# Performance work log

Measured on AMD Instinct MI355X. Metric: run time of the kernel, lower is better.

The kernel has to match this reference:

```python
import jax, jax.numpy as jnp
import numpy as np

B, T, I, H, O = 32, 2048, 12, 512, 3
L = 3  # GRU layers


def _gru_layer(x_seq, h0, w_ih, w_hh, b_ih, b_hh):
    # x_seq: [B,T,D], h0: [B,H]; PyTorch gate order: r, z, n
    xW = jnp.einsum('btd,gd->btg', x_seq, w_ih) + b_ih  # [B,T,3H]

    def step(h, xw_t):
        hw = h @ w_hh.T + b_hh                  # [B,3H]
        xr, xz, xn = jnp.split(xw_t, 3, axis=-1)
        hr, hz, hn = jnp.split(hw, 3, axis=-1)
        r = jax.nn.sigmoid(xr + hr)
        z = jax.nn.sigmoid(xz + hz)
        n = jnp.tanh(xn + r * hn)
        h_new = (1.0 - z) * n + z * h
        return h_new, h_new

    h_last, ys = jax.lax.scan(step, h0, jnp.swapaxes(xW, 0, 1))  # ys: [T,B,H]
    return jnp.swapaxes(ys, 0, 1), h_last


def _prelu(x, a):
    return jnp.where(x >= 0, x, a * x)


def setup_inputs() -> dict:
    key = jax.random.key(0)
    ks = jax.random.split(key, 40)
    s = 1.0 / np.sqrt(H)

    def u(k, shape):
        return jax.random.uniform(k, shape, jnp.float32, -s, s)

    inp = {
        'x': jax.random.normal(ks[0], (B, T, I), jnp.float32),
        'vel_init': jax.random.normal(ks[1], (B, 1, 3), jnp.float32),
    }
    in_dims = [I, H, H]
    for l in range(L):
        inp[f'w_ih_{l}'] = u(ks[2 + 4 * l], (3 * H, in_dims[l]))
        inp[f'w_hh_{l}'] = u(ks[3 + 4 * l], (3 * H, H))
        inp[f'b_ih_{l}'] = u(ks[4 + 4 * l], (3 * H,))
        inp[f'b_hh_{l}'] = u(ks[5 + 4 * l], (3 * H,))
    inp['a1'] = jnp.array([0.25], jnp.float32)  # PReLU (single shared param)
    inp['dec_in_w'] = u(ks[14], (H, I)); inp['dec_in_b'] = u(ks[15], (H,))
    inp['vd0_w'] = u(ks[16], (H, 3)); inp['vd0_b'] = u(ks[17], (H,))
    inp['vd1_w'] = u(ks[18], (H, 3)); inp['vd1_b'] = u(ks[19], (H,))
    inp['vd2_w'] = u(ks[20], (H, 3)); inp['vd2_b'] = u(ks[21], (H,))
    inp['vel_w'] = u(ks[22], (O, H)); inp['vel_b'] = u(ks[23], (O,))
    inp['std_w'] = u(ks[24], (O, H)); inp['std_b'] = u(ks[25], (O,))
    inp['attn_w'] = u(ks[26], (1, H)); inp['attn_b'] = u(ks[27], (1,))
    return inp


def reference(x, vel_init, w_ih_0, w_hh_0, b_ih_0, b_hh_0,
              w_ih_1, w_hh_1, b_ih_1, b_hh_1,
              w_ih_2, w_hh_2, b_ih_2, b_hh_2,
              a1, dec_in_w, dec_in_b,
              vd0_w, vd0_b, vd1_w, vd1_b, vd2_w, vd2_b,
              vel_w, vel_b, std_w, std_b, attn_w, attn_b):
    v0 = vel_init[:, 0, :]  # [B,3]
    # h0 per layer from velocity decoders (permute(1,0,2)+cat -> layer axis)
    h0s = [v0 @ vd0_w.T + vd0_b, v0 @ vd1_w.T + vd1_b, v0 @ vd2_w.T + vd2_b]
    w_ih = [w_ih_0, w_ih_1, w_ih_2]
    w_hh = [w_hh_0, w_hh_1, w_hh_2]
    b_ih = [b_ih_0, b_ih_1, b_ih_2]
    b_hh = [b_hh_0, b_hh_1, b_hh_2]

    out = x
    for l in range(L):
        out, _ = _gru_layer(out, h0s[l], w_ih[l], w_hh[l], b_ih[l], b_hh[l])

    out = _prelu(out, a1)
    # softmax skip-attention over time dim
    scores = jnp.einsum('bth,oh->bto', out, attn_w) + attn_b      # [B,T,1]
    attn = jax.nn.softmax(scores, axis=1)
    out = out + attn * (jnp.einsum('bti,hi->bth', x, dec_in_w) + dec_in_b)

    vel = jnp.einsum('bth,oh->bto', out, vel_w) + vel_b
    std = jnp.einsum('bth,oh->bto', out, std_w) + std_b
    return vel, std
```

## Files before the change

### kernel.cpp

```cpp
#include <hip/hip_runtime.h>
#include <stdint.h>


#define B_ 32
#define T_ 2048
#define H_ 512
#define R_ 128

typedef __attribute__((ext_vector_type(8))) short s8v;
typedef __attribute__((ext_vector_type(4))) float f4v;
typedef __attribute__((ext_vector_type(4))) uint32_t u32x4;
typedef __attribute__((ext_vector_type(2))) unsigned short u16x2;

__device__ __forceinline__ uint16_t f2bf(float f){ return __builtin_bit_cast(uint16_t, (__bf16)f); }
__device__ __forceinline__ float bf2f(uint16_t b){ return __builtin_bit_cast(float, ((uint32_t)b)<<16); }

__device__ __forceinline__ s8v pack8(const float* f){
  s8v r;
  #pragma unroll
  for (int i=0;i<8;++i) r[i] = (short)f2bf(f[i]);
  return r;
}
__device__ __forceinline__ f4v mfma16(s8v a, s8v b, f4v c){
  return __builtin_amdgcn_mfma_f32_16x16x32_bf16(a,b,c,0,0,0);
}
#if __has_builtin(__builtin_amdgcn_rcpf)
__device__ __forceinline__ float rcp_(float x){ return __builtin_amdgcn_rcpf(x); }
#else
__device__ __forceinline__ float rcp_(float x){ return 1.0f/x; }
#endif
__device__ __forceinline__ float sigm(float s){ return rcp_(1.f + __expf(-s)); }
__device__ __forceinline__ float tanh2(float v){ return 1.f - 2.f*rcp_(1.f + __expf(2.f*v)); }

__device__ __forceinline__ u32x4 load_x4_sc(const void* p){
  u32x4 r;
  asm volatile("global_load_dwordx4 %0, %1, off sc0 sc1" : "=v"(r) : "v"(p) : "memory");
  return r;
}
__device__ __forceinline__ uint32_t load_u32_sc_wait(const void* p){
  uint32_t r;
  asm volatile("global_load_dword %0, %1, off sc0 sc1\n\ts_waitcnt vmcnt(0)"
               : "=v"(r) : "v"(p) : "memory");
  return r;
}
__device__ __forceinline__ void store_s16_sc(void* p, uint32_t v){
  asm volatile("global_store_short %0, %1, off sc0 sc1" :: "v"(p), "v"(v) : "memory");
}
__device__ __forceinline__ void store_u32_sc(void* p, uint32_t v){
  asm volatile("global_store_dword %0, %1, off sc0 sc1" :: "v"(p), "v"(v) : "memory");
}

__device__ __forceinline__ bool valid16(const u32x4* a){
  u16x2 m = {0, 0};
  #pragma unroll
  for (int c=0;c<16;++c){
    #pragma unroll
    for (int i=0;i<4;++i)
      m = __builtin_elementwise_max(m, __builtin_bit_cast(u16x2, a[c][i]));
  }
  unsigned short mm = (m[0] > m[1]) ? m[0] : m[1];
  return mm != (unsigned short)0xFFFFu;
}

__global__ void poison_kernel(uint32_t* p, unsigned int n16)
{
  u32x4 v = {0xFFFFFFFFu, 0xFFFFFFFFu, 0xFFFFFFFFu, 0xFFFFFFFFu};
  for (unsigned int k = blockIdx.x*blockDim.x + threadIdx.x; k < n16;
       k += gridDim.x*blockDim.x)
    ((u32x4*)p)[k] = v;
}

__global__ void init_kernel(const float* __restrict__ vel_init,
    const float* __restrict__ w0, const float* __restrict__ b0,
    const float* __restrict__ w1, const float* __restrict__ b1,
    const float* __restrict__ w2, const float* __restrict__ b2,
    float* __restrict__ h0f, uint16_t* __restrict__ h0b, uint32_t* progress)
{
  const int l = blockIdx.x, tid = threadIdx.x;
  const float* w  = (l==0)?w0:((l==1)?w1:w2);
  const float* bb = (l==0)?b0:((l==1)?b1:b2);
  for (int idx = tid; idx < B_*H_; idx += 256){
    int b = idx >> 9, j = idx & 511;
    float s = bb[j] + vel_init[b*3+0]*w[j*3+0] + vel_init[b*3+1]*w[j*3+1]
                    + vel_init[b*3+2]*w[j*3+2];
    h0f[(size_t)l*(B_*H_) + idx] = s;
    h0b[(size_t)l*(B_*H_) + idx] = f2bf(s);
  }
  if (l == 0 && tid < 192) progress[tid] = 0;
}

struct ScanParams {
  const float* x;
  const float* wih[3];
  const float* whh[3];
  const float* bih[3];
  const float* bhh[3];
  const float* h0f;
  const uint16_t* h0b;
  uint16_t* ring0;
  uint16_t* ring1;
  uint16_t* out2;
  uint32_t* progress;
};

__global__ __launch_bounds__(128, 1) void fused_scan(ScanParams P)
{
  const int tid  = threadIdx.x;
  const int lane = tid & 63;
  const int mt   = tid >> 6;
  const int wgid = blockIdx.x;
  const int layer = wgid >> 5;
  const int wg   = wgid & 31;
  const int j0   = wg * 16;
  const int u    = lane & 15;
  const int lq   = lane >> 4;
  const int ko   = lq * 8;
  const int bd   = lq * 4;

  __shared__ uint16_t lds[48*512];

  const float* wih = P.wih[layer];
  const float* whh = P.whh[layer];
  const float* bih = P.bih[layer];
  const float* bhh = P.bhh[layer];

  const float bs0 = bih[0*H_ + j0 + u] + bhh[0*H_ + j0 + u];
  const float bs1 = bih[1*H_ + j0 + u] + bhh[1*H_ + j0 + u];
  const float bi2 = bih[2*H_ + j0 + u];
  const float bh2 = bhh[2*H_ + j0 + u];

  s8v whhf[3][16];
  #pragma unroll
  for (int nt=0; nt<3; ++nt){
    #pragma unroll
    for (int ks=0; ks<16; ++ks){
      const float* wp = whh + (size_t)(nt*H_ + j0 + u)*H_ + ks*32 + ko;
      float tmp[8];
      #pragma unroll
      for (int i=0;i<8;++i) tmp[i] = wp[i];
      whhf[nt][ks] = pack8(tmp);
    }
  }

  s8v w0f[3];
  if (layer == 0){
    #pragma unroll
    for (int nt=0; nt<3; ++nt){
      float tmp[8];
      #pragma unroll
      for (int i=0;i<8;++i){
        int k = ko + i;
        tmp[i] = (k < 12) ? wih[(size_t)(nt*H_ + j0 + u)*12 + k] : 0.f;
      }
      w0f[nt] = pack8(tmp);
    }
  } else {
    for (int e = tid; e < (48*512)/8; e += 128) {
      int idx = e * 8;
      int g = idx >> 9, k = idx & 511;
      const float* wp = wih + (size_t)((g>>4)*H_ + j0 + (g&15))*H_ + k;
      float tmp[8];
      #pragma unroll
      for (int i=0;i<8;++i) tmp[i] = wp[i];
      s8v v = pack8(tmp);
      uint32_t msk = (uint32_t)((((g&7) ^ (((g>>3)&1)<<1))) << 4);
      uint32_t off = (uint32_t)g*1024u + ((((uint32_t)k)*2u) ^ msk);
      *(u32x4*)((char*)lds + off) = __builtin_bit_cast(u32x4, v);
    }
  }
  __syncthreads();

  const uint16_t* inring = (layer==1) ? P.ring0 : P.ring1;
  uint16_t* outbuf = (layer==0) ? P.ring0 : ((layer==1) ? P.ring1 : P.out2);
  const bool outlin = (layer == 2);
  uint32_t* myprog = P.progress + layer*64 + wg*2 + mt;
  const uint32_t* nextprog = (layer<2) ? (P.progress + (layer+1)*64) : nullptr;

  float hold[4];
  #pragma unroll
  for (int r=0;r<4;++r)
    hold[r] = P.h0f[(size_t)layer*(B_*H_) + (size_t)(mt*16 + bd + r)*H_ + j0 + u];

  const uint32_t sw  = (uint32_t)((((u&7) ^ (((u>>3)&1)<<1))) << 4);
  const uint32_t gb0 = (uint32_t)((0*16 + u) * 1024);
  const uint32_t gb1 = (uint32_t)((1*16 + u) * 1024);
  const uint32_t gb2 = (uint32_t)((2*16 + u) * 1024);
  const uint32_t koB = (uint32_t)(ko * 2);

  int poison_until = R_/2 + 60;

  for (int t = 0; t < T_; ++t) {
    f4v ac0 = {0,0,0,0}, ac1 = {0,0,0,0}, axn = {0,0,0,0}, ahn = {0,0,0,0};

    if (layer == 0) {
      const float* xp = P.x + ((size_t)(mt*16 + u)*T_ + (size_t)t)*12;
      float4 lo  = *(const float4*)(xp);
      float4 md  = *(const float4*)(xp + 4);
      float4 hi4 = *(const float4*)(xp + 8);
      float xv[8];
      xv[0] = (ko==0) ? lo.x : hi4.x;  xv[1] = (ko==0) ? lo.y : hi4.y;
      xv[2] = (ko==0) ? lo.z : hi4.z;  xv[3] = (ko==0) ? lo.w : hi4.w;
      xv[4] = (ko==0) ? md.x : 0.f;    xv[5] = (ko==0) ? md.y : 0.f;
      xv[6] = (ko==0) ? md.z : 0.f;    xv[7] = (ko==0) ? md.w : 0.f;
      s8v a = pack8(xv);
      ac0 = mfma16(a, w0f[0], ac0);
      ac1 = mfma16(a, w0f[1], ac1);
      axn = mfma16(a, w0f[2], axn);
    }

    if (layer < 2 && t >= R_/2) {
      if (t > poison_until) {
        while (1) {
          int c = (int)load_u32_sc_wait(nextprog + lane);
          #pragma unroll
          for (int off=32; off>0; off>>=1){
            int c2 = __shfl_xor(c, off, 64);
            c = (c2 < c) ? c2 : c;
          }
          poison_until = c + R_/2 - 4;
          if (t <= poison_until) break;
          __builtin_amdgcn_s_sleep(8);
        }
      }
      int sp = (t + R_/2) & (R_-1);
      uint16_t* prow = outbuf + (size_t)sp*(B_*H_) + (size_t)(mt*16 + bd)*H_ + j0 + u;
      #pragma unroll
      for (int r=0;r<4;++r) store_s16_sc(prow + (size_t)r*H_, 0xFFFFu);
    }

    if (layer > 0 && (t & 15) == 15 && lane == 0)
      store_u32_sc(myprog, (uint32_t)t);

    u32x4 xa[16], ha[16];
    bool xok = (layer == 0);
    bool hok = (t == 0);
    const uint16_t* hp = ((t == 0)
        ? (P.h0b + (size_t)layer*(B_*H_))
        : (outlin ? (P.out2 + (size_t)(t-1)*(B_*H_))
                  : (outbuf + (size_t)((t-1) & (R_-1))*(B_*H_))))
        + (size_t)(mt*16+u)*H_ + ko;
    const uint16_t* xin = (layer > 0)
        ? (inring + (size_t)(t & (R_-1))*(B_*H_) + (size_t)(mt*16+u)*H_ + ko)
        : nullptr;

    #pragma unroll
    for (int ks=0; ks<16; ++ks) ha[ks] = load_x4_sc(hp + ks*32);
    if (layer > 0) {
      #pragma unroll
      for (int ks=0; ks<16; ++ks) xa[ks] = load_x4_sc(xin + ks*32);
    }
    asm volatile("s_waitcnt vmcnt(0)" ::: "memory");
    __builtin_amdgcn_sched_barrier(0);
    if (!hok) hok = (__ballot(valid16(ha)) == ~0ull);
    if (!xok) xok = (__ballot(valid16(xa)) == ~0ull);

    while (!xok) {
      #pragma unroll
      for (int ks=0; ks<16; ++ks) xa[ks] = load_x4_sc(xin + ks*32);
      if (!hok) {
        #pragma unroll
        for (int ks=0; ks<16; ++ks) ha[ks] = load_x4_sc(hp + ks*32);
      }
      asm volatile("s_waitcnt vmcnt(0)" ::: "memory");
      __builtin_amdgcn_sched_barrier(0);
      xok = (__ballot(valid16(xa)) == ~0ull);
      if (!hok) hok = (__ballot(valid16(ha)) == ~0ull);
    }

    if (layer > 0) {
      #pragma unroll
      for (int ks=0; ks<16; ++ks){
        s8v a = __builtin_bit_cast(s8v, xa[ks]);
        uint32_t kk = ((uint32_t)(ks*64) + koB) ^ sw;
        s8v w0 = *(const s8v*)((const char*)lds + gb0 + kk);
        s8v w1 = *(const s8v*)((const char*)lds + gb1 + kk);
        s8v w2 = *(const s8v*)((const char*)lds + gb2 + kk);
        ac0 = mfma16(a, w0, ac0);
        ac1 = mfma16(a, w1, ac1);
        axn = mfma16(a, w2, axn);
      }
    }

    while (!hok) {
      #pragma unroll
      for (int ks=0; ks<16; ++ks) ha[ks] = load_x4_sc(hp + ks*32);
      asm volatile("s_waitcnt vmcnt(0)" ::: "memory");
      __builtin_amdgcn_sched_barrier(0);
      hok = (__ballot(valid16(ha)) == ~0ull);
    }

    #pragma unroll
    for (int ks=0; ks<16; ++ks){
      s8v a = __builtin_bit_cast(s8v, ha[ks]);
      ac0 = mfma16(a, whhf[0][ks], ac0);
      ac1 = mfma16(a, whhf[1][ks], ac1);
      ahn = mfma16(a, whhf[2][ks], ahn);
    }

    uint16_t* orow = outbuf
        + (outlin ? (size_t)t*(B_*H_) : (size_t)(t & (R_-1))*(B_*H_))
        + (size_t)(mt*16 + bd)*H_ + j0 + u;
    #pragma unroll
    for (int r=0;r<4;++r){
      float rg = sigm(ac0[r] + bs0);
      float zg = sigm(ac1[r] + bs1);
      float ng = tanh2(axn[r] + bi2 + rg*(ahn[r] + bh2));
      float hv = ng + zg*(hold[r] - ng);
      hold[r] = hv;
      store_s16_sc(orow + (size_t)r*H_, (uint32_t)f2bf(hv));
    }
  }
}

__global__ void scores_kernel(const uint16_t* __restrict__ out2,
    const float* __restrict__ attn_w, const float* __restrict__ attn_b,
    const float* __restrict__ a1, float* __restrict__ scores)
{
  int gw = (blockIdx.x * blockDim.x + threadIdx.x) >> 6;
  int lane = threadIdx.x & 63;
  int b = gw >> 11, t = gw & 2047;
  float alpha = a1[0];
  u32x4 q = *(const u32x4*)(out2 + ((size_t)t*B_ + b)*H_ + lane*8);
  const uint16_t* ob = (const uint16_t*)&q;
  const float* aw = attn_w + lane*8;
  float acc = 0.f;
  #pragma unroll
  for (int i=0;i<8;++i){
    float ov = bf2f(ob[i]);
    ov = (ov >= 0.f) ? ov : alpha*ov;
    acc += ov * aw[i];
  }
  #pragma unroll
  for (int off=32; off>0; off>>=1) acc += __shfl_xor(acc, off, 64);
  if (lane == 0) scores[(size_t)b*T_ + t] = acc + attn_b[0];
}

__global__ void softmax_kernel(const float* __restrict__ scores, float* __restrict__ attn)
{
  int b = blockIdx.x, tid = threadIdx.x;
  __shared__ float red[256];
  const float* row = scores + (size_t)b*T_;
  float v[8]; float m = -3.4e38f;
  #pragma unroll
  for (int i=0;i<8;++i){ v[i] = row[tid + i*256]; m = fmaxf(m, v[i]); }
  red[tid] = m; __syncthreads();
  for (int s=128; s>0; s>>=1){ if (tid < s) red[tid] = fmaxf(red[tid], red[tid+s]); __syncthreads(); }
  m = red[0]; __syncthreads();
  float sum = 0.f;
  #pragma unroll
  for (int i=0;i<8;++i){ v[i] = __expf(v[i]-m); sum += v[i]; }
  red[tid] = sum; __syncthreads();
  for (int s=128; s>0; s>>=1){ if (tid < s) red[tid] += red[tid+s]; __syncthreads(); }
  float inv = 1.f / red[0];
  #pragma unroll
  for (int i=0;i<8;++i) attn[(size_t)b*T_ + tid + i*256] = v[i]*inv;
}

__global__ void final_kernel(const uint16_t* __restrict__ out2, const float* __restrict__ x,
    const float* __restrict__ attn, const float* __restrict__ dw, const float* __restrict__ db,
    const float* __restrict__ vw, const float* __restrict__ vb,
    const float* __restrict__ swt, const float* __restrict__ sb,
    const float* __restrict__ a1, float* __restrict__ dout)
{
  int gw = (blockIdx.x * blockDim.x + threadIdx.x) >> 6;
  int lane = threadIdx.x & 63;
  int b = gw >> 11, t = gw & 2047;
  float alpha = a1[0];
  u32x4 q = *(const u32x4*)(out2 + ((size_t)t*B_ + b)*H_ + lane*8);
  const uint16_t* ob = (const uint16_t*)&q;
  const float* xp = x + ((size_t)b*T_ + t)*12;
  float xr[12];
  #pragma unroll
  for (int i=0;i<12;++i) xr[i] = xp[i];
  float av = attn[(size_t)b*T_ + t];
  float acc[6] = {0,0,0,0,0,0};
  #pragma unroll
  for (int k=0;k<8;++k){
    int j = lane*8 + k;
    float ov = bf2f(ob[k]);
    ov = (ov >= 0.f) ? ov : alpha*ov;
    float d = db[j];
    const float* dwp = dw + (size_t)j*12;
    #pragma unroll
    for (int i=0;i<12;++i) d += xr[i]*dwp[i];
    float uo = ov + av*d;
    #pragma unroll
    for (int o=0;o<3;++o){
      acc[o]   += uo * vw[(size_t)o*H_ + j];
      acc[3+o] += uo * swt[(size_t)o*H_ + j];
    }
  }
  #pragma unroll
  for (int o=0;o<6;++o){
    #pragma unroll
    for (int off=32; off>0; off>>=1) acc[o] += __shfl_xor(acc[o], off, 64);
  }
  if (lane == 0){
    size_t p = ((size_t)b*T_ + t)*3;
    #pragma unroll
    for (int o=0;o<3;++o){
      dout[p + o] = acc[o] + vb[o];
      dout[(size_t)B_*T_*3 + p + o] = acc[3+o] + sb[o];
    }
  }
}

extern "C" void kernel_launch(void* const* d_in, const int* in_sizes, int n_in,
                              void* d_out, int out_size, void* d_ws, size_t ws_size,
                              hipStream_t stream)
{
  (void)in_sizes; (void)n_in; (void)out_size; (void)ws_size;
  const float* x        = (const float*)d_in[0];
  const float* vel_init = (const float*)d_in[1];
  const float* w_ih[3] = {(const float*)d_in[2], (const float*)d_in[6],  (const float*)d_in[10]};
  const float* w_hh[3] = {(const float*)d_in[3], (const float*)d_in[7],  (const float*)d_in[11]};
  const float* b_ih[3] = {(const float*)d_in[4], (const float*)d_in[8],  (const float*)d_in[12]};
  const float* b_hh[3] = {(const float*)d_in[5], (const float*)d_in[9],  (const float*)d_in[13]};
  const float* a1     = (const float*)d_in[14];
  const float* dec_w  = (const float*)d_in[15];
  const float* dec_b  = (const float*)d_in[16];
  const float* vd_w[3] = {(const float*)d_in[17], (const float*)d_in[19], (const float*)d_in[21]};
  const float* vd_b[3] = {(const float*)d_in[18], (const float*)d_in[20], (const float*)d_in[22]};
  const float* vel_w  = (const float*)d_in[23];
  const float* vel_b  = (const float*)d_in[24];
  const float* std_w  = (const float*)d_in[25];
  const float* std_b  = (const float*)d_in[26];
  const float* attn_w = (const float*)d_in[27];
  const float* attn_b = (const float*)d_in[28];

  char* ws = (char*)d_ws;
  uint16_t* out2   = (uint16_t*)(ws);
  uint16_t* ring0  = (uint16_t*)(ws + (size_t)67108864);
  uint16_t* ring1  = (uint16_t*)(ws + (size_t)71303168);
  float*    h0f    = (float*)   (ws + (size_t)75497472);
  uint16_t* h0b    = (uint16_t*)(ws + (size_t)75694080);
  float*    scores = (float*)   (ws + (size_t)75792384);
  float*    attnp  = (float*)   (ws + (size_t)76054528);
  uint32_t* progress = (uint32_t*)(ws + (size_t)76316672);

  poison_kernel<<<2048, 256, 0, stream>>>((uint32_t*)ws, 72u*1024u*1024u/16u);
  init_kernel<<<3, 256, 0, stream>>>(vel_init, vd_w[0], vd_b[0], vd_w[1], vd_b[1],
                                     vd_w[2], vd_b[2], h0f, h0b, progress);

  ScanParams P;
  P.x = x;
  for (int l=0;l<3;++l){ P.wih[l]=w_ih[l]; P.whh[l]=w_hh[l]; P.bih[l]=b_ih[l]; P.bhh[l]=b_hh[l]; }
  P.h0f = h0f; P.h0b = h0b;
  P.ring0 = ring0; P.ring1 = ring1; P.out2 = out2; P.progress = progress;

  fused_scan<<<96, 128, 0, stream>>>(P);

  scores_kernel<<<(B_*T_)/4, 256, 0, stream>>>(out2, attn_w, attn_b, a1, scores);
  softmax_kernel<<<B_, 256, 0, stream>>>(scores, attnp);
  final_kernel<<<(B_*T_)/4, 256, 0, stream>>>(out2, x, attnp, dec_w, dec_b,
                                              vel_w, vel_b, std_w, std_b, a1, (float*)d_out);
}
```

Baseline: 10.44 ms.

## Restructure GRU step polling: canary-chunk spin waits and move poisoning after compute

The per-step synchronisation of the persistent multi-layer GRU kernel is reorganised. The x-input wait now completes and feeds its MFMAs before the recurrent-state load starts. When a full 16-chunk load is invalid, each wave spins on a single 16-byte canary chunk per lane, with a short sleep, instead of reloading all 16 chunks. The ring-slot poisoning and progress publishing move after the gate compute and store, so they leave the critical path, and the initial poison threshold is lowered. This is meant to cut polling bandwidth and step latency, but the x and h loads are no longer overlapped and a canary can pass while other chunks are still stale, which costs an extra full reload.

```diff
diff --git a/kernel.cpp b/kernel.cpp
--- a/kernel.cpp
+++ b/kernel.cpp
@@ -37,6 +37,12 @@
   asm volatile("global_load_dwordx4 %0, %1, off sc0 sc1" : "=v"(r) : "v"(p) : "memory");
   return r;
 }
+__device__ __forceinline__ u32x4 load_x4_sc_wait(const void* p){
+  u32x4 r;
+  asm volatile("global_load_dwordx4 %0, %1, off sc0 sc1\n\ts_waitcnt vmcnt(0)"
+               : "=v"(r) : "v"(p) : "memory");
+  return r;
+}
 __device__ __forceinline__ uint32_t load_u32_sc_wait(const void* p){
   uint32_t r;
   asm volatile("global_load_dword %0, %1, off sc0 sc1\n\ts_waitcnt vmcnt(0)"
@@ -50,6 +56,14 @@
   asm volatile("global_store_dword %0, %1, off sc0 sc1" :: "v"(p), "v"(v) : "memory");
 }
 
+__device__ __forceinline__ bool chunk_ok(u32x4 c){
+  u16x2 m = __builtin_bit_cast(u16x2, c[0]);
+  m = __builtin_elementwise_max(m, __builtin_bit_cast(u16x2, c[1]));
+  m = __builtin_elementwise_max(m, __builtin_bit_cast(u16x2, c[2]));
+  m = __builtin_elementwise_max(m, __builtin_bit_cast(u16x2, c[3]));
+  unsigned short mm = (m[0] > m[1]) ? m[0] : m[1];
+  return mm != (unsigned short)0xFFFFu;
+}
 __device__ __forceinline__ bool valid16(const u32x4* a){
   u16x2 m = {0, 0};
   #pragma unroll
@@ -186,8 +200,9 @@
   const uint32_t gb1 = (uint32_t)((1*16 + u) * 1024);
   const uint32_t gb2 = (uint32_t)((2*16 + u) * 1024);
   const uint32_t koB = (uint32_t)(ko * 2);
-
-  int poison_until = R_/2 + 60;
+  const int cl = lane & 31;
+
+  int poison_until = R_/2 - 4;
 
   for (int t = 0; t < T_; ++t) {
     f4v ac0 = {0,0,0,0}, ac1 = {0,0,0,0}, axn = {0,0,0,0}, ahn = {0,0,0,0};
@@ -206,7 +221,79 @@
       ac0 = mfma16(a, w0f[0], ac0);
       ac1 = mfma16(a, w0f[1], ac1);
       axn = mfma16(a, w0f[2], axn);
-    }
+    } else {
+      const uint16_t* xslot = inring + (size_t)(t & (R_-1))*(B_*H_);
+      const uint16_t* xin  = xslot + (size_t)(mt*16+u)*H_ + ko;
+      const uint16_t* xcan = xslot + (size_t)(mt*16)*H_ + cl*16;
+      u32x4 xa[16];
+      while (1) {
+        #pragma unroll
+        for (int ks=0; ks<16; ++ks) xa[ks] = load_x4_sc(xin + ks*32);
+        asm volatile("s_waitcnt vmcnt(0)" ::: "memory");
+        __builtin_amdgcn_sched_barrier(0);
+        if (__ballot(valid16(xa)) == ~0ull) break;
+        while (1) {
+          u32x4 c = load_x4_sc_wait(xcan);
+          if (__ballot(chunk_ok(c)) == ~0ull) break;
+          __builtin_amdgcn_s_sleep(2);
+        }
+      }
+      #pragma unroll
+      for (int ks=0; ks<16; ++ks){
+        s8v a = __builtin_bit_cast(s8v, xa[ks]);
+        uint32_t kk = ((uint32_t)(ks*64) + koB) ^ sw;
+        s8v w0 = *(const s8v*)((const char*)lds + gb0 + kk);
+        s8v w1 = *(const s8v*)((const char*)lds + gb1 + kk);
+        s8v w2 = *(const s8v*)((const char*)lds + gb2 + kk);
+        ac0 = mfma16(a, w0, ac0);
+        ac1 = mfma16(a, w1, ac1);
+        axn = mfma16(a, w2, axn);
+      }
+    }
+
+    const uint16_t* hslot = (t == 0)
+        ? (P.h0b + (size_t)layer*(B_*H_))
+        : (outlin ? (P.out2 + (size_t)(t-1)*(B_*H_))
+                  : (outbuf + (size_t)((t-1) & (R_-1))*(B_*H_)));
+    const uint16_t* hp   = hslot + (size_t)(mt*16+u)*H_ + ko;
+    const uint16_t* hcan = hslot + (size_t)(mt*16)*H_ + cl*16;
+    u32x4 ha[16];
+    while (1) {
+      #pragma unroll
+      for (int ks=0; ks<16; ++ks) ha[ks] = load_x4_sc(hp + ks*32);
+      asm volatile("s_waitcnt vmcnt(0)" ::: "memory");
+      __builtin_amdgcn_sched_barrier(0);
+      if (t == 0) break;
+      if (__ballot(valid16(ha)) == ~0ull) break;
+      while (1) {
+        u32x4 c = load_x4_sc_wait(hcan);
+        if (__ballot(chunk_ok(c)) == ~0ull) break;
+        __builtin_amdgcn_s_sleep(2);
+      }
+    }
+    #pragma unroll
+    for (int ks=0; ks<16; ++ks){
+      s8v a = __builtin_bit_cast(s8v, ha[ks]);
+      ac0 = mfma16(a, whhf[0][ks], ac0);
+      ac1 = mfma16(a, whhf[1][ks], ac1);
+      ahn = mfma16(a, whhf[2][ks], ahn);
+    }
+
+    uint16_t* orow = outbuf
+        + (outlin ? (size_t)t*(B_*H_) : (size_t)(t & (R_-1))*(B_*H_))
+        + (size_t)(mt*16 + bd)*H_ + j0 + u;
+    #pragma unroll
+    for (int r=0;r<4;++r){
+      float rg = sigm(ac0[r] + bs0);
+      float zg = sigm(ac1[r] + bs1);
+      float ng = tanh2(axn[r] + bi2 + rg*(ahn[r] + bh2));
+      float hv = ng + zg*(hold[r] - ng);
+      hold[r] = hv;
+      store_s16_sc(orow + (size_t)r*H_, (uint32_t)f2bf(hv));
+    }
+
+    if (layer > 0 && (t & 15) == 15 && lane == 0)
+      store_u32_sc(myprog, (uint32_t)t);
 
     if (layer < 2 && t >= R_/2) {
       if (t > poison_until) {
@@ -226,88 +313,6 @@
       uint16_t* prow = outbuf + (size_t)sp*(B_*H_) + (size_t)(mt*16 + bd)*H_ + j0 + u;
       #pragma unroll
       for (int r=0;r<4;++r) store_s16_sc(prow + (size_t)r*H_, 0xFFFFu);
-    }
-
-    if (layer > 0 && (t & 15) == 15 && lane == 0)
-      store_u32_sc(myprog, (uint32_t)t);
-
-    u32x4 xa[16], ha[16];
-    bool xok = (layer == 0);
-    bool hok = (t == 0);
-    const uint16_t* hp = ((t == 0)
-        ? (P.h0b + (size_t)layer*(B_*H_))
-        : (outlin ? (P.out2 + (size_t)(t-1)*(B_*H_))
-                  : (outbuf + (size_t)((t-1) & (R_-1))*(B_*H_))))
-        + (size_t)(mt*16+u)*H_ + ko;
-    const uint16_t* xin = (layer > 0)
-        ? (inring + (size_t)(t & (R_-1))*(B_*H_) + (size_t)(mt*16+u)*H_ + ko)
-        : nullptr;
-
-    #pragma unroll
-    for (int ks=0; ks<16; ++ks) ha[ks] = load_x4_sc(hp + ks*32);
-    if (layer > 0) {
-      #pragma unroll
-      for (int ks=0; ks<16; ++ks) xa[ks] = load_x4_sc(xin + ks*32);
-    }
-    asm volatile("s_waitcnt vmcnt(0)" ::: "memory");
-    __builtin_amdgcn_sched_barrier(0);
-    if (!hok) hok = (__ballot(valid16(ha)) == ~0ull);
-    if (!xok) xok = (__ballot(valid16(xa)) == ~0ull);
-
-    while (!xok) {
-      #pragma unroll
-      for (int ks=0; ks<16; ++ks) xa[ks] = load_x4_sc(xin + ks*32);
-      if (!hok) {
-        #pragma unroll
-        for (int ks=0; ks<16; ++ks) ha[ks] = load_x4_sc(hp + ks*32);
-      }
-      asm volatile("s_waitcnt vmcnt(0)" ::: "memory");
-      __builtin_amdgcn_sched_barrier(0);
-      xok = (__ballot(valid16(xa)) == ~0ull);
-      if (!hok) hok = (__ballot(valid16(ha)) == ~0ull);
-    }
-
-    if (layer > 0) {
-      #pragma unroll
-      for (int ks=0; ks<16; ++ks){
-        s8v a = __builtin_bit_cast(s8v, xa[ks]);
-        uint32_t kk = ((uint32_t)(ks*64) + koB) ^ sw;
-        s8v w0 = *(const s8v*)((const char*)lds + gb0 + kk);
-        s8v w1 = *(const s8v*)((const char*)lds + gb1 + kk);
-        s8v w2 = *(const s8v*)((const char*)lds + gb2 + kk);
-        ac0 = mfma16(a, w0, ac0);
-        ac1 = mfma16(a, w1, ac1);
-        axn = mfma16(a, w2, axn);
-      }
-    }
-
-    while (!hok) {
-      #pragma unroll
-      for (int ks=0; ks<16; ++ks) ha[ks] = load_x4_sc(hp + ks*32);
-      asm volatile("s_waitcnt vmcnt(0)" ::: "memory");
-      __builtin_amdgcn_sched_barrier(0);
-      hok = (__ballot(valid16(ha)) == ~0ull);
-    }
-
-    #pragma unroll
-    for (int ks=0; ks<16; ++ks){
-      s8v a = __builtin_bit_cast(s8v, ha[ks]);
-      ac0 = mfma16(a, whhf[0][ks], ac0);
-      ac1 = mfma16(a, whhf[1][ks], ac1);
-      ahn = mfma16(a, whhf[2][ks], ahn);
-    }
-
-    uint16_t* orow = outbuf
-        + (outlin ? (size_t)t*(B_*H_) : (size_t)(t & (R_-1))*(B_*H_))
-        + (size_t)(mt*16 + bd)*H_ + j0 + u;
-    #pragma unroll
-    for (int r=0;r<4;++r){
-      float rg = sigm(ac0[r] + bs0);
-      float zg = sigm(ac1[r] + bs1);
-      float ng = tanh2(axn[r] + bi2 + rg*(ahn[r] + bh2));
-      float hv = ng + zg*(hold[r] - ng);
-      hold[r] = hv;
-      store_s16_sc(orow + (size_t)r*H_, (uint32_t)f2bf(hv));
     }
   }
 }
```

Result: faster. 8.427 ms (-19.3%).
